# Kernel tuning notes

Hardware: AMD Instinct MI355X
Metric: run time of the kernel (lower is better)

## Reference

```python
import jax, jax.numpy as jnp
import numpy as np

T, B, E, H = 2048, 2, 1024, 16
D = E // H
MAX_REL = 16  # RelativePosition default max_relative_position


def setup_inputs() -> dict:
    key = jax.random.key(0)
    ks = jax.random.split(key, 11)
    s = 1.0 / np.sqrt(E)
    inp = {
        'query': jax.random.normal(ks[0], (T, B, E), dtype=jnp.float32),
        'Wq': jax.random.normal(ks[1], (E, E), dtype=jnp.float32) * s,
        'bq': jnp.zeros((E,), dtype=jnp.float32),
        'Wk': jax.random.normal(ks[2], (E, E), dtype=jnp.float32) * s,
        'bk': jnp.zeros((E,), dtype=jnp.float32),
        'Wv': jax.random.normal(ks[3], (E, E), dtype=jnp.float32) * s,
        'bv': jnp.zeros((E,), dtype=jnp.float32),
        'Wo': jax.random.normal(ks[4], (E, E), dtype=jnp.float32) * s,
        'bo': jnp.zeros((E,), dtype=jnp.float32),
        'rk_table': jax.random.normal(ks[5], (2 * MAX_REL + 1, D), dtype=jnp.float32) * 0.05,
        'rv_table': jax.random.normal(ks[6], (2 * MAX_REL + 1, D), dtype=jnp.float32) * 0.05,
    }
    return inp


def _rel_idx(lq, lk):
    # distance_mat = k - q, clipped to [-MAX_REL, MAX_REL], shifted to [0, 2*MAX_REL]
    d = jnp.arange(lk)[None, :] - jnp.arange(lq)[:, None]
    return jnp.clip(d, -MAX_REL, MAX_REL) + MAX_REL  # [lq, lk] int


def reference(query, Wq, bq, Wk, bk, Wv, bv, Wo, bo, rk_table, rv_table):
    t, b, e = query.shape
    scale = D ** -0.5
    # projections (torch Linear: x @ W.T + b)
    q = (query @ Wq.T + bq) * scale
    k = query @ Wk.T + bk
    v = query @ Wv.T + bv
    # [T,B,E] -> [B*H, T, D]
    q = q.reshape(t, b * H, D).transpose(1, 0, 2)
    k = k.reshape(t, b * H, D).transpose(1, 0, 2)
    v = v.reshape(t, b * H, D).transpose(1, 0, 2)
    # content scores + Shaw relative-position key scores
    scores = jnp.einsum('ntd,nsd->nts', q, k)            # [N, T, S]
    rk = rk_table[_rel_idx(t, t)]                        # [T, S, D]
    scores = scores + jnp.einsum('ntd,tsd->nts', q, rk)  # relpos_k term
    probs = jax.nn.softmax(scores, axis=-1)
    # weighted values + Shaw relative-position value term
    rv = rv_table[_rel_idx(t, t)]                        # [T, S, D]
    attn = jnp.einsum('nts,nsd->ntd', probs, v) + jnp.einsum('nts,tsd->ntd', probs, rv)
    # [B*H, T, D] -> [T, B, E]
    attn = attn.transpose(1, 0, 2).reshape(t, b, e)
    return attn @ Wo.T + bo
```

## Files before the change

kernel.cpp:

```cpp
#include <hip/hip_runtime.h>
#include <hip/hip_bf16.h>
#include <math.h>

#define T_   2048
#define B_   2
#define E_   1024
#define H_   16
#define D_   64
#define NH_  32
#define M_   4096

typedef __attribute__((ext_vector_type(8))) short s8b;
typedef __attribute__((ext_vector_type(4))) float f4;

#define MFMA_B16(a,b,c) __builtin_amdgcn_mfma_f32_16x16x32_bf16(a,b,c,0,0,0)
#define LOG2E 1.44269504088896f

__device__ __forceinline__ unsigned short f2bu(float f) {
    union { __hip_bfloat16 h; unsigned short u; } cv;
    cv.h = __float2bfloat16(f);
    return cv.u;
}
__device__ __forceinline__ unsigned short f2bu_fast(float f) {
    return (unsigned short)((__float_as_uint(f) + 0x8000u) >> 16);
}
__device__ __forceinline__ float bu2f(unsigned short u) {
    union { __hip_bfloat16 h; unsigned short u; } cv; cv.u = u;
    return __bfloat162float(cv.h);
}
__device__ __forceinline__ unsigned int pk2(float a, float b) {
    return (unsigned int)f2bu(a) | ((unsigned int)f2bu(b) << 16);
}
__device__ __forceinline__ unsigned int pk2_fast(float a, float b) {
    return ((__float_as_uint(a) + 0x8000u) >> 16) |
           ((__float_as_uint(b) + 0x8000u) & 0xFFFF0000u);
}
__device__ __forceinline__ float fexp2(float x) {
    return __builtin_amdgcn_exp2f(x);
}
__device__ __forceinline__ float ld1d(const void* p, size_t idx, bool f32) {
    return f32 ? ((const float*)p)[idx] : bu2f(((const unsigned short*)p)[idx]);
}
__device__ __forceinline__ float qsumq(float v) {
    v += __shfl_xor(v, 16); v += __shfl_xor(v, 32);
    return v;
}
__device__ __forceinline__ void glds16(const unsigned short* g, unsigned short* l) {
    __builtin_amdgcn_global_load_lds(
        (const __attribute__((address_space(1))) unsigned int*)g,
        (__attribute__((address_space(3))) unsigned int*)l, 16, 0, 0);
}
__device__ __forceinline__ bool detect_f32(const unsigned short* q16) {
    int e = (q16[threadIdx.x & 63] >> 7) & 0xFF;
    bool sane = (e == 0) || (e >= 97 && e <= 157);
    unsigned long long m = __ballot(sane);
    return __popcll(m) < 56;
}

__global__ __launch_bounds__(256) void cvt_bf16(
    const void* __restrict__ x,
    const void* __restrict__ Wq, const void* __restrict__ Wk,
    const void* __restrict__ Wv, const void* __restrict__ Wo,
    const void* __restrict__ bq, const void* __restrict__ bk,
    const void* __restrict__ bv, const void* __restrict__ bo,
    unsigned short* __restrict__ xw, unsigned short* __restrict__ Ww,
    unsigned short* __restrict__ bw, int* __restrict__ flag)
{
    const bool f32m = detect_f32((const unsigned short*)x);
    if (blockIdx.x == 0 && blockIdx.y == 0 && threadIdx.x == 0)
        *flag = f32m ? 1 : 0;
    const int y = blockIdx.y;
    const void* src; unsigned short* dst; int n;
    if (y == 0)      { src = x; dst = xw; n = M_ * E_; }
    else if (y <= 4) {
        src = (y == 1) ? Wq : (y == 2) ? Wk : (y == 3) ? Wv : Wo;
        dst = Ww + (size_t)(y - 1) * E_ * E_; n = E_ * E_;
    } else {
        src = (y == 5) ? bq : (y == 6) ? bk : (y == 7) ? bv : bo;
        dst = bw + (size_t)(y - 5) * E_; n = E_;
    }
    int i = (blockIdx.x * 256 + threadIdx.x) * 8;
    if (i >= n) return;
    if (f32m) {
        const float* s = (const float*)src + i;
        float4 f0 = *(const float4*)s, f1 = *(const float4*)(s + 4);
        union { unsigned int d[4]; s8b v; } u;
        u.d[0] = pk2(f0.x, f0.y); u.d[1] = pk2(f0.z, f0.w);
        u.d[2] = pk2(f1.x, f1.y); u.d[3] = pk2(f1.z, f1.w);
        *(s8b*)(dst + i) = u.v;
    } else {
        *(s8b*)(dst + i) = *(const s8b*)((const unsigned short*)src + i);
    }
}

__global__ __launch_bounds__(256, 3) void qkv_gemm(
    const unsigned short* __restrict__ xw, const unsigned short* __restrict__ Ww,
    const unsigned short* __restrict__ bw,
    unsigned short* __restrict__ qo, unsigned short* __restrict__ ko,
    unsigned short* __restrict__ vo)
{
    const int bid = blockIdx.x;
    const int r_ = bid & 7, s_ = bid >> 3;
    const int g = r_ + 8 * (s_ >> 3);
    const int e0 = (s_ & 7) * 128;
    const int m0 = (g & 31) * 128;
    const int p  = g >> 5;
    const unsigned short* W    = Ww + (size_t)p * E_ * E_;
    const unsigned short* bias = bw + (size_t)p * E_;
    const float scale = (p == 0) ? 0.125f * LOG2E : 1.0f;

    const int tid = threadIdx.x, w = tid >> 6, lane = tid & 63;
    const int quad = lane >> 4, lc = lane & 15;
    const int wx = w & 1, wy = w >> 1;

    __shared__ unsigned short a_s[2][128 * 32];
    __shared__ unsigned short b_s[2][128 * 32];

    f4 acc[4][4];
    #pragma unroll
    for (int i = 0; i < 4; i++)
        #pragma unroll
        for (int j = 0; j < 4; j++) acc[i][j] = (f4){0.f, 0.f, 0.f, 0.f};

    const int gr = lane >> 2;
    const int gc = (lane & 3) ^ ((lane >> 2) & 3);
    const size_t aoff = (size_t)(m0 + w*32 + gr) * E_ + gc*8;
    const size_t boff = (size_t)(e0 + w*32 + gr) * E_ + gc*8;

    #pragma unroll
    for (int j = 0; j < 2; j++) {
        glds16(xw + aoff + (size_t)j*16*E_, &a_s[0][(w*128 + j*64) * 8]);
        glds16(W  + boff + (size_t)j*16*E_, &b_s[0][(w*128 + j*64) * 8]);
    }
    __syncthreads();

    const int fcA = quad ^ (lc & 3);
    for (int k0 = 0; k0 < E_; k0 += 32) {
        const int cur = (k0 >> 5) & 1;
        if (k0 + 32 < E_) {
            #pragma unroll
            for (int j = 0; j < 2; j++) {
                glds16(xw + aoff + (size_t)j*16*E_ + k0 + 32, &a_s[cur^1][(w*128 + j*64) * 8]);
                glds16(W  + boff + (size_t)j*16*E_ + k0 + 32, &b_s[cur^1][(w*128 + j*64) * 8]);
            }
        }
        s8b af[4], bfr[4];
        #pragma unroll
        for (int i = 0; i < 4; i++)
            af[i]  = *(const s8b*)&a_s[cur][((wy*64 + i*16 + lc)*4 + fcA) * 8];
        #pragma unroll
        for (int i = 0; i < 4; i++)
            bfr[i] = *(const s8b*)&b_s[cur][((wx*64 + i*16 + lc)*4 + fcA) * 8];
        #pragma unroll
        for (int ms = 0; ms < 4; ms++)
            #pragma unroll
            for (int ns = 0; ns < 4; ns++)
                acc[ms][ns] = MFMA_B16(af[ms], bfr[ns], acc[ms][ns]);
        __syncthreads();
    }

    float bias_v[4];
    #pragma unroll
    for (int ns = 0; ns < 4; ns++) bias_v[ns] = bu2f(bias[e0 + wx*64 + ns*16 + lc]);

    if (p < 2) {
        #pragma unroll
        for (int ms = 0; ms < 4; ms++)
            #pragma unroll
            for (int ns = 0; ns < 4; ns++)
                #pragma unroll
                for (int r2 = 0; r2 < 4; r2++) {
                    float val = (acc[ms][ns][r2] + bias_v[ns]) * scale;
                    float nb = __shfl_xor(val, 1);
                    if (!(lane & 1)) {
                        int m = m0 + wy*64 + ms*16 + quad*4 + r2;
                        int t = m >> 1, bb = m & 1;
                        int e = e0 + wx*64 + ns*16 + lc;
                        int h = e >> 6, d = e & 63;
                        unsigned short* dst = (p == 0) ? qo : ko;
                        *(unsigned int*)&dst[(((size_t)(bb*H_ + h) * T_ + t) << 6) + d] = pk2(val, nb);
                    }
                }
    } else {
        #pragma unroll
        for (int ms = 0; ms < 4; ms++) {
            int t0v = (m0 + wy*64 + ms*16 + quad*4) >> 1;
            #pragma unroll
            for (int ns = 0; ns < 4; ns++) {
                int e = e0 + wx*64 + ns*16 + lc;
                int h = e >> 6, d = e & 63;
                float v0 = acc[ms][ns][0] + bias_v[ns];
                float v1 = acc[ms][ns][1] + bias_v[ns];
                float v2 = acc[ms][ns][2] + bias_v[ns];
                float v3 = acc[ms][ns][3] + bias_v[ns];
                *(unsigned int*)&vo[((size_t)h        * 64 + d) * T_ + t0v] = pk2(v0, v2);
                *(unsigned int*)&vo[((size_t)(H_ + h) * 64 + d) * T_ + t0v] = pk2(v1, v3);
            }
        }
    }
}

__global__ __launch_bounds__(256, 2) void attn_mfma(
    const unsigned short* __restrict__ q, const unsigned short* __restrict__ k,
    const unsigned short* __restrict__ v,
    const void* __restrict__ rk_t, const void* __restrict__ rv_t,
    unsigned short* __restrict__ aout, const int* __restrict__ flag)
{
    const bool f32m = (*flag != 0);
    const int bid = blockIdx.x;
    const int n = bid & 31, qt = bid >> 5;
    const int t0 = qt * 128;
    const int tid = threadIdx.x, w = tid >> 6, lane = tid & 63;
    const int quad = lane >> 4, lc = lane & 15;

    __shared__ unsigned short k_s[2][64 * 64];
    __shared__ unsigned short v_s[2][64 * 64];
    __shared__ unsigned short p_s[4][32 * 72];
    __shared__ unsigned short qrk_s[128 * 36];
    __shared__ unsigned short diag16[128 * 33];
    __shared__ float st_L[128], st_R[128];

    const unsigned short* qn = q + ((size_t)n * T_ + t0) * D_;
    const unsigned short* kn = k + (size_t)n * T_ * D_;
    const unsigned short* vn = v + (size_t)n * D_ * T_;

    s8b qa[2][2];
    #pragma unroll
    for (int nt = 0; nt < 2; nt++)
        #pragma unroll
        for (int kf = 0; kf < 2; kf++)
            qa[nt][kf] = *(const s8b*)(qn + (size_t)(w*32 + nt*16 + lc) * D_ + kf*32 + quad*8);

    for (int i = tid; i < 128 * 33; i += 256) diag16[i] = 0;

    unsigned int* rks = (unsigned int*)&p_s[0][0];
    for (int i = tid; i < 48 * 36; i += 256) {
        int r = i / 36, c2 = i % 36;
        unsigned int val = 0;
        if (r < 33 && c2 < 32)
            val = pk2(ld1d(rk_t, r*64 + 2*c2, f32m), ld1d(rk_t, r*64 + 2*c2 + 1, f32m));
        rks[i] = val;
    }
    __syncthreads();

    #pragma unroll
    for (int mt = 0; mt < 2; mt++)
        for (int nt = 0; nt < 3; nt++) {
            s8b b0 = *(const s8b*)((const unsigned short*)rks + (nt*16 + lc)*72 + quad*8);
            s8b b1 = *(const s8b*)((const unsigned short*)rks + (nt*16 + lc)*72 + 32 + quad*8);
            f4 a = (f4){0.f, 0.f, 0.f, 0.f};
            a = MFMA_B16(qa[mt][0], b0, a);
            a = MFMA_B16(qa[mt][1], b1, a);
            #pragma unroll
            for (int r = 0; r < 4; r++) {
                float nb = __shfl_xor(a[r], 1);
                int col = nt*16 + lc;
                if (!(lane & 1) && col < 34)
                    ((unsigned int*)qrk_s)[(w*32 + mt*16 + quad*4 + r)*18 + (col >> 1)] = pk2(a[r], nb);
            }
        }
    __syncthreads();

    float qLn[2], qRn[2];
    float L_p[2] = {0.f, 0.f}, R_p[2] = {0.f, 0.f};
    f4 O[4][2], lsN[2], lsL[2], lsR[2];
    #pragma unroll
    for (int nt = 0; nt < 2; nt++) {
        int row = w*32 + nt*16 + lc;
        qLn[nt] = bu2f(qrk_s[row*36 + 0]);
        qRn[nt] = bu2f(qrk_s[row*36 + 32]);
        lsN[nt] = (f4){0.f, 0.f, 0.f, 0.f};
        lsL[nt] = (f4){0.f, 0.f, 0.f, 0.f};
        lsR[nt] = (f4){0.f, 0.f, 0.f, 0.f};
        #pragma unroll
        for (int dt = 0; dt < 4; dt++) O[dt][nt] = (f4){0.f, 0.f, 0.f, 0.f};
    }
    const short ob = (short)0x3F80;
    const s8b ones = { ob, ob, ob, ob, ob, ob, ob, ob };

    const int grr = lane >> 3;
    const int gcc = (lane & 7) ^ grr;
    const size_t koff = (size_t)(w*16 + grr) * D_ + gcc*8;
    const size_t voff = (size_t)(w*16 + grr) * T_ + gcc*8;

    s8b kr0 = *(const s8b*)(kn + koff);
    s8b kr1 = *(const s8b*)(kn + koff + 8*D_);
    s8b vr0 = *(const s8b*)(vn + voff);
    s8b vr1 = *(const s8b*)(vn + voff + (size_t)8*T_);
    *(s8b*)&k_s[0][(w*128 +      lane) * 8] = kr0;
    *(s8b*)&k_s[0][(w*128 + 64 + lane) * 8] = kr1;
    *(s8b*)&v_s[0][(w*128 +      lane) * 8] = vr0;
    *(s8b*)&v_s[0][(w*128 + 64 + lane) * 8] = vr1;
    __syncthreads();

    const int lc7 = lc & 7;
    for (int kt = 0; kt < 32; kt++) {
        const int s0 = kt * 64;
        const int cur = kt & 1;
        if (kt + 1 < 32) {
            kr0 = *(const s8b*)(kn + koff + (size_t)(s0 + 64)*D_);
            kr1 = *(const s8b*)(kn + koff + (size_t)(s0 + 72)*D_);
            vr0 = *(const s8b*)(vn + voff + s0 + 64);
            vr1 = *(const s8b*)(vn + voff + (size_t)8*T_ + s0 + 64);
        }

        const bool farL  = (s0 + 63 < t0 - 16);
        const bool farR  = (s0 > t0 + 143);
        const bool nearT = !farL && !farR;

        s8b ak[4][2];
        #pragma unroll
        for (int st = 0; st < 4; st++) {
            int row = st*16 + lc;
            ak[st][0] = *(const s8b*)&k_s[cur][(row*8 + (quad       ^ lc7)) * 8];
            ak[st][1] = *(const s8b*)&k_s[cur][(row*8 + ((4 + quad) ^ lc7)) * 8];
        }

        #pragma unroll
        for (int st = 0; st < 4; st++)
            #pragma unroll
            for (int nt = 0; nt < 2; nt++) {
                f4 a;
                if (nearT) a = (f4){0.f, 0.f, 0.f, 0.f};
                else {
                    float qb = farL ? qLn[nt] : qRn[nt];
                    a = (f4){qb, qb, qb, qb};
                }
                a = MFMA_B16(ak[st][0], qa[nt][0], a);
                a = MFMA_B16(ak[st][1], qa[nt][1], a);
                unsigned int lo, hi;
                if (nearT) {
                    const int t_l = w*32 + nt*16 + lc;
                    const int sb  = s0 + st*16 + quad*4 - (t0 + t_l);
                    unsigned short eb[4];
                    #pragma unroll
                    for (int r = 0; r < 4; r++) {
                        int rel = sb + r;
                        int rc = rel < -16 ? -16 : (rel > 16 ? 16 : rel);
                        float e = fexp2(a[r] + bu2f(qrk_s[t_l*36 + rc + 16]));
                        eb[r] = f2bu_fast(e);
                        if (rel <= -16)      L_p[nt] += e;
                        else if (rel >= 16)  R_p[nt] += e;
                        else                 diag16[t_l*33 + rel + 15] = eb[r];
                    }
                    lo = (unsigned int)eb[0] | ((unsigned int)eb[1] << 16);
                    hi = (unsigned int)eb[2] | ((unsigned int)eb[3] << 16);
                } else {
                    lo = pk2_fast(fexp2(a[0]), fexp2(a[1]));
                    hi = pk2_fast(fexp2(a[2]), fexp2(a[3]));
                }
                *(uint2*)&p_s[w][(nt*16 + lc)*72 + st*16 + quad*4] = make_uint2(lo, hi);
            }

        s8b pb[2][2];
        #pragma unroll
        for (int nt = 0; nt < 2; nt++) {
            pb[nt][0] = *(const s8b*)&p_s[w][(nt*16 + lc)*72 + quad*8];
            pb[nt][1] = *(const s8b*)&p_s[w][(nt*16 + lc)*72 + 32 + quad*8];
        }
        if (nearT) {
            #pragma unroll
            for (int nt = 0; nt < 2; nt++) {
                lsN[nt] = MFMA_B16(ones, pb[nt][0], lsN[nt]);
                lsN[nt] = MFMA_B16(ones, pb[nt][1], lsN[nt]);
            }
        } else if (farL) {
            #pragma unroll
            for (int nt = 0; nt < 2; nt++) {
                lsL[nt] = MFMA_B16(ones, pb[nt][0], lsL[nt]);
                lsL[nt] = MFMA_B16(ones, pb[nt][1], lsL[nt]);
            }
        } else {
            #pragma unroll
            for (int nt = 0; nt < 2; nt++) {
                lsR[nt] = MFMA_B16(ones, pb[nt][0], lsR[nt]);
                lsR[nt] = MFMA_B16(ones, pb[nt][1], lsR[nt]);
            }
        }
        #pragma unroll
        for (int dt = 0; dt < 4; dt++) {
            int row = dt*16 + lc;
            s8b a0 = *(const s8b*)&v_s[cur][(row*8 + (quad       ^ lc7)) * 8];
            s8b a1 = *(const s8b*)&v_s[cur][(row*8 + ((4 + quad) ^ lc7)) * 8];
            O[dt][0] = MFMA_B16(a0, pb[0][0], O[dt][0]);
            O[dt][0] = MFMA_B16(a1, pb[0][1], O[dt][0]);
            O[dt][1] = MFMA_B16(a0, pb[1][0], O[dt][1]);
            O[dt][1] = MFMA_B16(a1, pb[1][1], O[dt][1]);
        }

        if (kt + 1 < 32) {
            *(s8b*)&k_s[cur ^ 1][(w*128 +      lane) * 8] = kr0;
            *(s8b*)&k_s[cur ^ 1][(w*128 + 64 + lane) * 8] = kr1;
            *(s8b*)&v_s[cur ^ 1][(w*128 +      lane) * 8] = vr0;
            *(s8b*)&v_s[cur ^ 1][(w*128 + 64 + lane) * 8] = vr1;
        }
        __syncthreads();
    }

    float linv[2];
    #pragma unroll
    for (int nt = 0; nt < 2; nt++) {
        float l = lsN[nt][0] + lsL[nt][0] + lsR[nt][0];
        float L = lsL[nt][0] + qsumq(L_p[nt]);
        float R = lsR[nt][0] + qsumq(R_p[nt]);
        linv[nt] = 1.f / l;
        if (quad == 0) {
            int row = w*32 + nt*16 + lc;
            st_L[row] = L; st_R[row] = R;
        }
    }
    {
        unsigned int* rvs = (unsigned int*)&k_s[0][0];
        for (int i = tid; i < 64 * 32; i += 256) {
            int d = i >> 5, dwL = i & 31;
            int r0 = dwL * 2, r1 = r0 + 1;
            float x0 = (r0 < 33) ? ld1d(rv_t, (size_t)r0 * 64 + d, f32m) : 0.f;
            float x1 = (r1 < 33) ? ld1d(rv_t, (size_t)r1 * 64 + d, f32m) : 0.f;
            int phys = d * 32 + ((dwL >> 2) ^ (d & 7)) * 4 + (dwL & 3);
            rvs[phys] = pk2(x0, x1);
        }
    }
    __syncthreads();
    for (int j = 0; j < 32; j++) {
        int c = lane;
        int row = w*32 + j;
        unsigned short pv;
        if (c == 0)        pv = f2bu(st_L[row]);
        else if (c == 32)  pv = f2bu(st_R[row]);
        else if (c < 32)   pv = diag16[row*33 + c - 1];
        else               pv = 0;
        p_s[w][j*72 + c] = pv;
    }
    s8b pe[2][2];
    #pragma unroll
    for (int nt = 0; nt < 2; nt++) {
        pe[nt][0] = *(const s8b*)&p_s[w][(nt*16 + lc)*72 + quad*8];
        pe[nt][1] = *(const s8b*)&p_s[w][(nt*16 + lc)*72 + 32 + quad*8];
    }
    #pragma unroll
    for (int dt = 0; dt < 4; dt++) {
        int row = dt*16 + lc;
        s8b a0 = *(const s8b*)&k_s[0][(row*8 + (quad       ^ lc7)) * 8];
        s8b a1 = *(const s8b*)&k_s[0][(row*8 + ((4 + quad) ^ lc7)) * 8];
        O[dt][0] = MFMA_B16(a0, pe[0][0], O[dt][0]);
        O[dt][0] = MFMA_B16(a1, pe[0][1], O[dt][0]);
        O[dt][1] = MFMA_B16(a0, pe[1][0], O[dt][1]);
        O[dt][1] = MFMA_B16(a1, pe[1][1], O[dt][1]);
    }
    const int bb = n >> 4, h = n & 15;
    #pragma unroll
    for (int nt = 0; nt < 2; nt++) {
        int t_g = t0 + w*32 + nt*16 + lc;
        #pragma unroll
        for (int dt = 0; dt < 4; dt++) {
            float v0 = O[dt][nt][0] * linv[nt];
            float v1 = O[dt][nt][1] * linv[nt];
            float v2 = O[dt][nt][2] * linv[nt];
            float v3 = O[dt][nt][3] * linv[nt];
            int e = h*64 + dt*16 + quad*4;
            *(uint2*)&aout[((size_t)t_g * B_ + bb) * E_ + e] =
                make_uint2(pk2(v0, v1), pk2(v2, v3));
        }
    }
}

__global__ __launch_bounds__(256, 3) void out_gemm(
    const unsigned short* __restrict__ A,
    const unsigned short* __restrict__ Wob, const unsigned short* __restrict__ bob,
    void* __restrict__ out, const int* __restrict__ flag)
{
    const bool f32m = (*flag != 0);
    const int bid = blockIdx.x;
    const int r_ = bid & 7, s_ = bid >> 3;
    const int g = r_ + 8 * (s_ >> 3);
    const int m0 = g * 128;
    const int e0 = (s_ & 7) * 128;

    const int tid = threadIdx.x, w = tid >> 6, lane = tid & 63;
    const int quad = lane >> 4, lc = lane & 15;
    const int wx = w & 1, wy = w >> 1;

    __shared__ unsigned short a_s[2][128 * 32];
    __shared__ unsigned short b_s[2][128 * 32];

    f4 acc[4][4];
    #pragma unroll
    for (int i = 0; i < 4; i++)
        #pragma unroll
        for (int j = 0; j < 4; j++) acc[i][j] = (f4){0.f, 0.f, 0.f, 0.f};

    const int gr = lane >> 2;
    const int gc = (lane & 3) ^ ((lane >> 2) & 3);
    const size_t aoff = (size_t)(m0 + w*32 + gr) * E_ + gc*8;
    const size_t boff = (size_t)(e0 + w*32 + gr) * E_ + gc*8;

    #pragma unroll
    for (int j = 0; j < 2; j++) {
        glds16(A   + aoff + (size_t)j*16*E_, &a_s[0][(w*128 + j*64) * 8]);
        glds16(Wob + boff + (size_t)j*16*E_, &b_s[0][(w*128 + j*64) * 8]);
    }
    __syncthreads();

    const int fcA = quad ^ (lc & 3);
    for (int k0 = 0; k0 < E_; k0 += 32) {
        const int cur = (k0 >> 5) & 1;
        if (k0 + 32 < E_) {
            #pragma unroll
            for (int j = 0; j < 2; j++) {
                glds16(A   + aoff + (size_t)j*16*E_ + k0 + 32, &a_s[cur^1][(w*128 + j*64) * 8]);
                glds16(Wob + boff + (size_t)j*16*E_ + k0 + 32, &b_s[cur^1][(w*128 + j*64) * 8]);
            }
        }
        s8b af[4], bfr[4];
        #pragma unroll
        for (int i = 0; i < 4; i++)
            af[i]  = *(const s8b*)&a_s[cur][((wy*64 + i*16 + lc)*4 + fcA) * 8];
        #pragma unroll
        for (int i = 0; i < 4; i++)
            bfr[i] = *(const s8b*)&b_s[cur][((wx*64 + i*16 + lc)*4 + fcA) * 8];
        #pragma unroll
        for (int ms = 0; ms < 4; ms++)
            #pragma unroll
            for (int ns = 0; ns < 4; ns++)
                acc[ms][ns] = MFMA_B16(af[ms], bfr[ns], acc[ms][ns]);
        __syncthreads();
    }

    float bias_v[4];
    #pragma unroll
    for (int ns = 0; ns < 4; ns++) bias_v[ns] = bu2f(bob[e0 + wx*64 + ns*16 + lc]);

    #pragma unroll
    for (int ms = 0; ms < 4; ms++)
        #pragma unroll
        for (int ns = 0; ns < 4; ns++)
            #pragma unroll
            for (int r2 = 0; r2 < 4; r2++) {
                float val = acc[ms][ns][r2] + bias_v[ns];
                size_t m = m0 + wy*64 + ms*16 + quad*4 + r2;
                int e = e0 + wx*64 + ns*16 + lc;
                if (f32m) {
                    ((float*)out)[m * E_ + e] = val;
                } else {
                    float nb = __shfl_xor(val, 1);
                    if (!(lane & 1))
                        *(unsigned int*)&((unsigned short*)out)[m * E_ + e] = pk2(val, nb);
                }
            }
}

extern "C" void kernel_launch(void* const* d_in, const int* in_sizes, int n_in,
                              void* d_out, int out_size, void* d_ws, size_t ws_size,
                              hipStream_t stream) {
    const void* x  = d_in[0];
    const void* Wq = d_in[1];  const void* bq = d_in[2];
    const void* Wk = d_in[3];  const void* bk = d_in[4];
    const void* Wv = d_in[5];  const void* bv = d_in[6];
    const void* Wo = d_in[7];  const void* bo = d_in[8];
    const void* rk = d_in[9];  const void* rv = d_in[10];

    int* flag = (int*)d_ws;
    const size_t HTD = (size_t)NH_ * T_ * D_;
    unsigned short* qw = (unsigned short*)((char*)d_ws + 256);
    unsigned short* kw = qw + HTD;
    unsigned short* vw = kw + HTD;
    unsigned short* aw = vw + HTD;
    unsigned short* xw = aw + (size_t)M_ * E_;
    unsigned short* Ww = xw + (size_t)M_ * E_;
    unsigned short* bw = Ww + (size_t)4 * E_ * E_;

    cvt_bf16<<<dim3((M_*E_/8 + 255)/256, 9), 256, 0, stream>>>(
        x, Wq, Wk, Wv, Wo, bq, bk, bv, bo, xw, Ww, bw, flag);
    qkv_gemm<<<dim3(768), 256, 0, stream>>>(xw, Ww, bw, qw, kw, vw);
    attn_mfma<<<dim3(NH_ * (T_/128)), 256, 0, stream>>>(qw, kw, vw, rk, rv, aw, flag);
    out_gemm<<<dim3(256), 256, 0, stream>>>(aw, Ww + (size_t)3*E_*E_, bw + 3*E_,
                                            d_out, flag);
}
```

Measured before the change: 234.7 us.

## Load K/V tiles directly from global into registers, dropping LDS staging

Replaces the LDS double-buffered K/V staging and per-tile __syncthreads with direct per-wave global loads of MFMA operand fragments. K for the next tile is prefetched into a ping-pong register set through an unrolled lambda, and V is loaded for the current tile. This removes the block barriers and shared-memory traffic, and the rv table scratch reuses the qrk_s buffer. In exchange, each of the four waves reloads the full K/V tiles from global/L2, loads become less coalesced, and register pressure rises.

```diff
diff --git a/kernel.cpp b/kernel.cpp
--- a/kernel.cpp
+++ b/kernel.cpp
@@ -213,8 +213,6 @@
     const int tid = threadIdx.x, w = tid >> 6, lane = tid & 63;
     const int quad = lane >> 4, lc = lane & 15;
 
-    __shared__ unsigned short k_s[2][64 * 64];
-    __shared__ unsigned short v_s[2][64 * 64];
     __shared__ unsigned short p_s[4][32 * 72];
     __shared__ unsigned short qrk_s[128 * 36];
     __shared__ unsigned short diag16[128 * 33];
@@ -278,43 +276,26 @@
     const short ob = (short)0x3F80;
     const s8b ones = { ob, ob, ob, ob, ob, ob, ob, ob };
 
-    const int grr = lane >> 3;
-    const int gcc = (lane & 7) ^ grr;
-    const size_t koff = (size_t)(w*16 + grr) * D_ + gcc*8;
-    const size_t voff = (size_t)(w*16 + grr) * T_ + gcc*8;
-
-    s8b kr0 = *(const s8b*)(kn + koff);
-    s8b kr1 = *(const s8b*)(kn + koff + 8*D_);
-    s8b vr0 = *(const s8b*)(vn + voff);
-    s8b vr1 = *(const s8b*)(vn + voff + (size_t)8*T_);
-    *(s8b*)&k_s[0][(w*128 +      lane) * 8] = kr0;
-    *(s8b*)&k_s[0][(w*128 + 64 + lane) * 8] = kr1;
-    *(s8b*)&v_s[0][(w*128 +      lane) * 8] = vr0;
-    *(s8b*)&v_s[0][(w*128 + 64 + lane) * 8] = vr1;
-    __syncthreads();
-
     const int lc7 = lc & 7;
-    for (int kt = 0; kt < 32; kt++) {
+
+    auto tile_body = [&](s8b (&cK)[4][2], s8b (&nK)[4][2], int kt) {
         const int s0 = kt * 64;
-        const int cur = kt & 1;
-        if (kt + 1 < 32) {
-            kr0 = *(const s8b*)(kn + koff + (size_t)(s0 + 64)*D_);
-            kr1 = *(const s8b*)(kn + koff + (size_t)(s0 + 72)*D_);
-            vr0 = *(const s8b*)(vn + voff + s0 + 64);
-            vr1 = *(const s8b*)(vn + voff + (size_t)8*T_ + s0 + 64);
-        }
+        const int s0n = (kt < 31) ? s0 + 64 : s0;
+        #pragma unroll
+        for (int st = 0; st < 4; st++)
+            #pragma unroll
+            for (int kf = 0; kf < 2; kf++)
+                nK[st][kf] = *(const s8b*)(kn + (size_t)(s0n + st*16 + lc) * D_ + kf*32 + quad*8);
+        s8b cv[4][2];
+        #pragma unroll
+        for (int dt = 0; dt < 4; dt++)
+            #pragma unroll
+            for (int kf = 0; kf < 2; kf++)
+                cv[dt][kf] = *(const s8b*)(vn + (size_t)(dt*16 + lc) * T_ + s0 + kf*32 + quad*8);
 
         const bool farL  = (s0 + 63 < t0 - 16);
         const bool farR  = (s0 > t0 + 143);
         const bool nearT = !farL && !farR;
-
-        s8b ak[4][2];
-        #pragma unroll
-        for (int st = 0; st < 4; st++) {
-            int row = st*16 + lc;
-            ak[st][0] = *(const s8b*)&k_s[cur][(row*8 + (quad       ^ lc7)) * 8];
-            ak[st][1] = *(const s8b*)&k_s[cur][(row*8 + ((4 + quad) ^ lc7)) * 8];
-        }
 
         #pragma unroll
         for (int st = 0; st < 4; st++)
@@ -326,8 +307,8 @@
                     float qb = farL ? qLn[nt] : qRn[nt];
                     a = (f4){qb, qb, qb, qb};
                 }
-                a = MFMA_B16(ak[st][0], qa[nt][0], a);
-                a = MFMA_B16(ak[st][1], qa[nt][1], a);
+                a = MFMA_B16(cK[st][0], qa[nt][0], a);
+                a = MFMA_B16(cK[st][1], qa[nt][1], a);
                 unsigned int lo, hi;
                 if (nearT) {
                     const int t_l = w*32 + nt*16 + lc;
@@ -379,22 +360,23 @@
         }
         #pragma unroll
         for (int dt = 0; dt < 4; dt++) {
-            int row = dt*16 + lc;
-            s8b a0 = *(const s8b*)&v_s[cur][(row*8 + (quad       ^ lc7)) * 8];
-            s8b a1 = *(const s8b*)&v_s[cur][(row*8 + ((4 + quad) ^ lc7)) * 8];
-            O[dt][0] = MFMA_B16(a0, pb[0][0], O[dt][0]);
-            O[dt][0] = MFMA_B16(a1, pb[0][1], O[dt][0]);
-            O[dt][1] = MFMA_B16(a0, pb[1][0], O[dt][1]);
-            O[dt][1] = MFMA_B16(a1, pb[1][1], O[dt][1]);
-        }
-
-        if (kt + 1 < 32) {
-            *(s8b*)&k_s[cur ^ 1][(w*128 +      lane) * 8] = kr0;
-            *(s8b*)&k_s[cur ^ 1][(w*128 + 64 + lane) * 8] = kr1;
-            *(s8b*)&v_s[cur ^ 1][(w*128 +      lane) * 8] = vr0;
-            *(s8b*)&v_s[cur ^ 1][(w*128 + 64 + lane) * 8] = vr1;
-        }
-        __syncthreads();
+            O[dt][0] = MFMA_B16(cv[dt][0], pb[0][0], O[dt][0]);
+            O[dt][0] = MFMA_B16(cv[dt][1], pb[0][1], O[dt][0]);
+            O[dt][1] = MFMA_B16(cv[dt][0], pb[1][0], O[dt][1]);
+            O[dt][1] = MFMA_B16(cv[dt][1], pb[1][1], O[dt][1]);
+        }
+    };
+
+    s8b kA[4][2], kB[4][2];
+    #pragma unroll
+    for (int st = 0; st < 4; st++)
+        #pragma unroll
+        for (int kf = 0; kf < 2; kf++)
+            kA[st][kf] = *(const s8b*)(kn + (size_t)(st*16 + lc) * D_ + kf*32 + quad*8);
+
+    for (int kt2 = 0; kt2 < 32; kt2 += 2) {
+        tile_body(kA, kB, kt2);
+        tile_body(kB, kA, kt2 + 1);
     }
 
     float linv[2];
@@ -409,8 +391,9 @@
             st_L[row] = L; st_R[row] = R;
         }
     }
+    __syncthreads();
     {
-        unsigned int* rvs = (unsigned int*)&k_s[0][0];
+        unsigned int* rvs = (unsigned int*)&qrk_s[0];
         for (int i = tid; i < 64 * 32; i += 256) {
             int d = i >> 5, dwL = i & 31;
             int r0 = dwL * 2, r1 = r0 + 1;
@@ -440,8 +423,8 @@
     #pragma unroll
     for (int dt = 0; dt < 4; dt++) {
         int row = dt*16 + lc;
-        s8b a0 = *(const s8b*)&k_s[0][(row*8 + (quad       ^ lc7)) * 8];
-        s8b a1 = *(const s8b*)&k_s[0][(row*8 + ((4 + quad) ^ lc7)) * 8];
+        s8b a0 = *(const s8b*)&qrk_s[(row*8 + (quad       ^ lc7)) * 8];
+        s8b a1 = *(const s8b*)&qrk_s[(row*8 + ((4 + quad) ^ lc7)) * 8];
         O[dt][0] = MFMA_B16(a0, pe[0][0], O[dt][0]);
         O[dt][0] = MFMA_B16(a1, pe[0][1], O[dt][0]);
         O[dt][1] = MFMA_B16(a0, pe[1][0], O[dt][1]);
```

Result: slower. 299.4 us (+27.6%).

## Software-pipeline PV MFMA phase one key tile behind QK/softmax

Applied to the files above, without the earlier changes.

Restructures the attention key loop so the P·V and row-sum MFMAs for tile k-1 run during iteration k, after the QK scores and exponentials of tile k are computed. P fragments and V fragments are held in registers across iterations using A/B ping-pong buffers, with a prologue and epilogue. The goal is to overlap the exp/softmax VALU work with the MFMA work and hide LDS latency. The cost is higher register pressure from the extra fragment buffers, which may lower occupancy.

```diff
diff --git a/kernel.cpp b/kernel.cpp
--- a/kernel.cpp
+++ b/kernel.cpp
@@ -294,7 +294,42 @@
     __syncthreads();
 
     const int lc7 = lc & 7;
-    for (int kt = 0; kt < 32; kt++) {
+
+    s8b pbA[2][2], pbB[2][2];
+    s8b vcA[4][2], vcB[4][2];
+    int clsA = 0, clsB = 0;
+
+    auto pv_phase = [&](s8b (&pb)[2][2], s8b (&vc)[4][2], int cls) {
+        if (cls == 0) {
+            #pragma unroll
+            for (int nt = 0; nt < 2; nt++) {
+                lsN[nt] = MFMA_B16(ones, pb[nt][0], lsN[nt]);
+                lsN[nt] = MFMA_B16(ones, pb[nt][1], lsN[nt]);
+            }
+        } else if (cls == 1) {
+            #pragma unroll
+            for (int nt = 0; nt < 2; nt++) {
+                lsL[nt] = MFMA_B16(ones, pb[nt][0], lsL[nt]);
+                lsL[nt] = MFMA_B16(ones, pb[nt][1], lsL[nt]);
+            }
+        } else {
+            #pragma unroll
+            for (int nt = 0; nt < 2; nt++) {
+                lsR[nt] = MFMA_B16(ones, pb[nt][0], lsR[nt]);
+                lsR[nt] = MFMA_B16(ones, pb[nt][1], lsR[nt]);
+            }
+        }
+        #pragma unroll
+        for (int dt = 0; dt < 4; dt++) {
+            O[dt][0] = MFMA_B16(vc[dt][0], pb[0][0], O[dt][0]);
+            O[dt][0] = MFMA_B16(vc[dt][1], pb[0][1], O[dt][0]);
+            O[dt][1] = MFMA_B16(vc[dt][0], pb[1][0], O[dt][1]);
+            O[dt][1] = MFMA_B16(vc[dt][1], pb[1][1], O[dt][1]);
+        }
+    };
+
+    auto body = [&](int kt, s8b (&pbC)[2][2], s8b (&vcC)[4][2], int& clsC,
+                    s8b (&pbP)[2][2], s8b (&vcP)[4][2], int& clsP, bool doPV) {
         const int s0 = kt * 64;
         const int cur = kt & 1;
         if (kt + 1 < 32) {
@@ -307,6 +342,7 @@
         const bool farL  = (s0 + 63 < t0 - 16);
         const bool farR  = (s0 > t0 + 143);
         const bool nearT = !farL && !farR;
+        clsC = nearT ? 0 : (farL ? 1 : 2);
 
         s8b ak[4][2];
         #pragma unroll
@@ -352,40 +388,19 @@
                 *(uint2*)&p_s[w][(nt*16 + lc)*72 + st*16 + quad*4] = make_uint2(lo, hi);
             }
 
-        s8b pb[2][2];
-        #pragma unroll
-        for (int nt = 0; nt < 2; nt++) {
-            pb[nt][0] = *(const s8b*)&p_s[w][(nt*16 + lc)*72 + quad*8];
-            pb[nt][1] = *(const s8b*)&p_s[w][(nt*16 + lc)*72 + 32 + quad*8];
-        }
-        if (nearT) {
-            #pragma unroll
-            for (int nt = 0; nt < 2; nt++) {
-                lsN[nt] = MFMA_B16(ones, pb[nt][0], lsN[nt]);
-                lsN[nt] = MFMA_B16(ones, pb[nt][1], lsN[nt]);
-            }
-        } else if (farL) {
-            #pragma unroll
-            for (int nt = 0; nt < 2; nt++) {
-                lsL[nt] = MFMA_B16(ones, pb[nt][0], lsL[nt]);
-                lsL[nt] = MFMA_B16(ones, pb[nt][1], lsL[nt]);
-            }
-        } else {
-            #pragma unroll
-            for (int nt = 0; nt < 2; nt++) {
-                lsR[nt] = MFMA_B16(ones, pb[nt][0], lsR[nt]);
-                lsR[nt] = MFMA_B16(ones, pb[nt][1], lsR[nt]);
-            }
-        }
         #pragma unroll
         for (int dt = 0; dt < 4; dt++) {
             int row = dt*16 + lc;
-            s8b a0 = *(const s8b*)&v_s[cur][(row*8 + (quad       ^ lc7)) * 8];
-            s8b a1 = *(const s8b*)&v_s[cur][(row*8 + ((4 + quad) ^ lc7)) * 8];
-            O[dt][0] = MFMA_B16(a0, pb[0][0], O[dt][0]);
-            O[dt][0] = MFMA_B16(a1, pb[0][1], O[dt][0]);
-            O[dt][1] = MFMA_B16(a0, pb[1][0], O[dt][1]);
-            O[dt][1] = MFMA_B16(a1, pb[1][1], O[dt][1]);
+            vcC[dt][0] = *(const s8b*)&v_s[cur][(row*8 + (quad       ^ lc7)) * 8];
+            vcC[dt][1] = *(const s8b*)&v_s[cur][(row*8 + ((4 + quad) ^ lc7)) * 8];
+        }
+
+        if (doPV) pv_phase(pbP, vcP, clsP);
+
+        #pragma unroll
+        for (int nt = 0; nt < 2; nt++) {
+            pbC[nt][0] = *(const s8b*)&p_s[w][(nt*16 + lc)*72 + quad*8];
+            pbC[nt][1] = *(const s8b*)&p_s[w][(nt*16 + lc)*72 + 32 + quad*8];
         }
 
         if (kt + 1 < 32) {
@@ -395,7 +410,15 @@
             *(s8b*)&v_s[cur ^ 1][(w*128 + 64 + lane) * 8] = vr1;
         }
         __syncthreads();
-    }
+    };
+
+    body(0, pbA, vcA, clsA, pbB, vcB, clsB, false);
+    for (int kt2 = 1; kt2 < 31; kt2 += 2) {
+        body(kt2,     pbB, vcB, clsB, pbA, vcA, clsA, true);
+        body(kt2 + 1, pbA, vcA, clsA, pbB, vcB, clsB, true);
+    }
+    body(31, pbB, vcB, clsB, pbA, vcA, clsA, true);
+    pv_phase(pbB, vcB, clsB);
 
     float linv[2];
     #pragma unroll
```

After: 235.7 us. Within noise of the previous version (+0.4%).
